# Kernel optimization log

Hardware: AMD Instinct MI355X
Metric: run time of the kernel (lower is better)

Reference implementation:

```python
import jax, jax.numpy as jnp
import numpy as np

N_NODES = 100000
N_EDGES = 1600000
N_GRAPHS = 256
F_NODE, F_EDGE, HID, OUT = 64, 16, 128, 128
BN_SCALE = 1.0 / np.sqrt(1.0 + 1e-5)  # BatchNorm eval with running mean 0, var 1


def setup_inputs() -> dict:
    key = jax.random.key(0)
    ks = iter(jax.random.split(key, 64))
    inp = {}
    inp["x"] = jax.random.normal(next(ks), (N_NODES, F_NODE), dtype=jnp.float32)
    inp["edge_attr"] = jax.random.normal(next(ks), (N_EDGES, F_EDGE), dtype=jnp.float32)
    inp["edge_index"] = jax.random.randint(next(ks), (2, N_EDGES), 0, N_NODES)
    inp["batch"] = jnp.sort(jax.random.randint(next(ks), (N_NODES,), 0, N_GRAPHS))

    def p(shape, scale):
        return (jax.random.normal(next(ks), shape, dtype=jnp.float32) * scale)

    in_dims = [F_NODE, HID, HID]
    for i, d in enumerate(in_dims):
        inp[f"el_w{i}"] = p((F_EDGE, d), F_EDGE ** -0.5)
        inp[f"el_b{i}"] = jnp.zeros((d,), jnp.float32)
        inp[f"c{i}_w1"] = p((d, HID), d ** -0.5)
        inp[f"c{i}_b1"] = jnp.zeros((HID,), jnp.float32)
        inp[f"c{i}_g"] = jnp.ones((HID,), jnp.float32)
        inp[f"c{i}_bt"] = jnp.zeros((HID,), jnp.float32)
        inp[f"c{i}_w2"] = p((HID, HID), HID ** -0.5)
        inp[f"c{i}_b2"] = jnp.zeros((HID,), jnp.float32)
    inp["o_w1"] = p((HID, OUT), HID ** -0.5)
    inp["o_b1"] = jnp.zeros((OUT,), jnp.float32)
    inp["o_w2"] = p((OUT, OUT), OUT ** -0.5)
    inp["o_b2"] = jnp.zeros((OUT,), jnp.float32)
    return inp


def reference(x, edge_attr,
              el_w0, el_b0, c0_w1, c0_b1, c0_g, c0_bt, c0_w2, c0_b2,
              el_w1, el_b1, c1_w1, c1_b1, c1_g, c1_bt, c1_w2, c1_b2,
              el_w2, el_b2, c2_w1, c2_b1, c2_g, c2_bt, c2_w2, c2_b2,
              o_w1, o_b1, o_w2, o_b2,
              edge_index, batch):
    src, dst = edge_index[0], edge_index[1]
    n = x.shape[0]
    layers = [
        (el_w0, el_b0, c0_w1, c0_b1, c0_g, c0_bt, c0_w2, c0_b2),
        (el_w1, el_b1, c1_w1, c1_b1, c1_g, c1_bt, c1_w2, c1_b2),
        (el_w2, el_b2, c2_w1, c2_b1, c2_g, c2_bt, c2_w2, c2_b2),
    ]
    h = x
    for (ew, eb, w1, b1, g, bt, w2, b2) in layers:
        ea = edge_attr @ ew + eb                              # [E, d]
        msg = jax.nn.relu(h[src] + ea)                        # GINEConv message
        agg = jax.ops.segment_sum(msg, dst, num_segments=n)   # scatter-sum to targets
        hh = h + agg                                          # (1+eps)*x + aggr, eps=0
        hh = hh @ w1 + b1                                     # MLP: Linear
        hh = g * (hh * BN_SCALE) + bt                         # BatchNorm1d (eval)
        hh = jax.nn.relu(hh)
        hh = hh @ w2 + b2                                     # MLP: Linear
        h = jax.nn.relu(hh)                                   # dropout(p=0, eval) + act
    s = jax.ops.segment_sum(h, batch, num_segments=N_GRAPHS)
    cnt = jax.ops.segment_sum(jnp.ones((n,), h.dtype), batch, num_segments=N_GRAPHS)
    pooled = s / jnp.maximum(cnt, 1.0)[:, None]               # scatter-mean pooling
    out = jax.nn.relu(pooled @ o_w1 + o_b1) @ o_w2 + o_b2     # out_lin
    return out
```

## Files before the change

### kernel.cpp

```cpp
#include <hip/hip_runtime.h>
#include <hip/hip_fp16.h>
#include <cstdint>
#include <cstddef>

#define N_NODES_C  100000
#define N_EDGES_C  1600000
#define N_GRAPHS_C 256
#define HID_C      128
#define BN_SCALE_C 0.9999950000374997f

#define SCAN_B 1024
#define SCAN_NB ((N_NODES_C + SCAN_B - 1) / SCAN_B)

typedef _Float16 h2 __attribute__((ext_vector_type(2)));
typedef _Float16 h4 __attribute__((ext_vector_type(4)));
typedef _Float16 h8 __attribute__((ext_vector_type(8)));
typedef float    f4 __attribute__((ext_vector_type(4)));

struct __align__(16) EA8 { h2 p[4]; };
struct __align__(8)  HQ  { h2 a, b; };
struct __align__(16) H8  { __half2 v[4]; };

#if defined(__has_builtin)
#  if __has_builtin(__builtin_amdgcn_fdot2)
#    define HAVE_FDOT2 1
#  endif
#endif
#ifndef HAVE_FDOT2
#  define HAVE_FDOT2 0
#endif

__device__ __forceinline__ float fdot2_(h2 a, h2 b, float c)
{
#if HAVE_FDOT2
    return __builtin_amdgcn_fdot2(a, b, c, false);
#else
    return c + (float)a[0] * (float)b[0] + (float)a[1] * (float)b[1];
#endif
}

__global__ __launch_bounds__(256) void hist_kernel(
    const int* __restrict__ dst, int* __restrict__ counts, int n_edges)
{
    int e = blockIdx.x * 256 + threadIdx.x;
    if (e < n_edges) atomicAdd(&counts[dst[e]], 1);
}

__global__ __launch_bounds__(SCAN_B) void scan1_kernel(
    const int* __restrict__ counts, int* __restrict__ incl,
    int* __restrict__ blocksums, int n)
{
    __shared__ int sdata[SCAN_B];
    const int lid = threadIdx.x;
    const int i = blockIdx.x * SCAN_B + lid;
    sdata[lid] = (i < n) ? counts[i] : 0;
    __syncthreads();
#pragma unroll
    for (int off = 1; off < SCAN_B; off <<= 1) {
        int t = (lid >= off) ? sdata[lid - off] : 0;
        __syncthreads();
        sdata[lid] += t;
        __syncthreads();
    }
    if (i < n) incl[i] = sdata[lid];
    if (lid == SCAN_B - 1) blocksums[blockIdx.x] = sdata[lid];
}

__global__ void scan2_kernel(const int* __restrict__ blocksums,
                             int* __restrict__ blockoffs, int nb)
{
    if (threadIdx.x == 0 && blockIdx.x == 0) {
        int off = 0;
        for (int b = 0; b < nb; ++b) { blockoffs[b] = off; off += blocksums[b]; }
    }
}

__global__ __launch_bounds__(SCAN_B) void scan3_kernel(
    int* __restrict__ incl, const int* __restrict__ blockoffs, int n)
{
    const int i = blockIdx.x * SCAN_B + threadIdx.x;
    if (i < n) incl[i] += blockoffs[blockIdx.x];
}

__global__ __launch_bounds__(256) void initrows_kernel(
    const int* __restrict__ incl, const int* __restrict__ counts,
    int* __restrict__ rowstart, int* __restrict__ cursor, int n)
{
    const int i = blockIdx.x * 256 + threadIdx.x;
    if (i < n) {
        const int rs = incl[i] - counts[i];
        rowstart[i] = rs;
        cursor[i]   = rs;
    }
}

__global__ __launch_bounds__(256) void scatter_kernel(
    const int* __restrict__ src, const int* __restrict__ dst,
    int* __restrict__ cursor, int* __restrict__ perm_src,
    int* __restrict__ perm_eid, int n_edges)
{
    const int e = blockIdx.x * 256 + threadIdx.x;
    if (e < n_edges) {
        const int pos = atomicAdd(&cursor[dst[e]], 1);
        perm_src[pos] = src[e];
        perm_eid[pos] = e;
    }
}

__global__ __launch_bounds__(256) void permute_ea_f16_kernel(
    const float* __restrict__ edge_attr, const int* __restrict__ perm_eid,
    __half* __restrict__ ea_f16, int n_edges)
{
    const int j = blockIdx.x * 256 + threadIdx.x;
    if (j >= n_edges) return;
    const int eid = perm_eid[j];
    const float4* p = (const float4*)(edge_attr + (size_t)eid * 16);
    const float4 q0 = p[0], q1 = p[1], q2 = p[2], q3 = p[3];
    H8 a, b;
    a.v[0] = __floats2half2_rn(q0.x, q0.y);
    a.v[1] = __floats2half2_rn(q0.z, q0.w);
    a.v[2] = __floats2half2_rn(q1.x, q1.y);
    a.v[3] = __floats2half2_rn(q1.z, q1.w);
    b.v[0] = __floats2half2_rn(q2.x, q2.y);
    b.v[1] = __floats2half2_rn(q2.z, q2.w);
    b.v[2] = __floats2half2_rn(q3.x, q3.y);
    b.v[3] = __floats2half2_rn(q3.z, q3.w);
    H8* o = (H8*)(ea_f16 + (size_t)j * 16);
    o[0] = a;
    o[1] = b;
}

__global__ __launch_bounds__(256) void cast_f16_kernel(
    const float* __restrict__ in, _Float16* __restrict__ out, int n4)
{
    const int i = blockIdx.x * 256 + threadIdx.x;
    if (i >= n4) return;
    const float4 v = ((const float4*)in)[i];
    h4 o; o[0] = (_Float16)v.x; o[1] = (_Float16)v.y;
    o[2] = (_Float16)v.z; o[3] = (_Float16)v.w;
    *(h4*)(out + (size_t)i * 4) = o;
}

__global__ __launch_bounds__(256) void transpose_w_kernel(
    const float* __restrict__ w, _Float16* __restrict__ wt, int K, int N)
{
    const int i = blockIdx.x * 256 + threadIdx.x;
    if (i >= K * N) return;
    const int n = i / K;
    const int k = i - n * K;
    wt[(size_t)n * K + k] = (_Float16)w[(size_t)k * N + n];
}

__device__ __forceinline__ float4 eamlp2(const EA8 a0, const EA8 c0,
                                         const h2 (*ew2h)[4], const float4 ebv)
{
    float4 m = {ebv.x, ebv.y, ebv.z, ebv.w};
#pragma unroll
    for (int k = 0; k < 4; ++k) {
        m.x = fdot2_(a0.p[k], ew2h[k][0], m.x);
        m.y = fdot2_(a0.p[k], ew2h[k][1], m.y);
        m.z = fdot2_(a0.p[k], ew2h[k][2], m.z);
        m.w = fdot2_(a0.p[k], ew2h[k][3], m.w);
    }
#pragma unroll
    for (int k = 0; k < 4; ++k) {
        m.x = fdot2_(c0.p[k], ew2h[4 + k][0], m.x);
        m.y = fdot2_(c0.p[k], ew2h[4 + k][1], m.y);
        m.z = fdot2_(c0.p[k], ew2h[4 + k][2], m.z);
        m.w = fdot2_(c0.p[k], ew2h[4 + k][3], m.w);
    }
    return m;
}

template<int DIN>
__global__ __launch_bounds__(256) void gine_agg_kernel(
    const _Float16* __restrict__ hin, const _Float16* __restrict__ ea16,
    const int* __restrict__ perm_src,
    const int* __restrict__ rowstart, const int* __restrict__ rowend,
    const float* __restrict__ ew, const float* __restrict__ eb,
    _Float16* __restrict__ x16, int n_nodes)
{
    constexpr int NQ    = DIN / 4;
    constexpr int SLOTS = 256 / NQ;
    const int fq   = threadIdx.x & (NQ - 1);
    const int slot = threadIdx.x / NQ;
    const int v = blockIdx.x * SLOTS + slot;
    if (v >= n_nodes) return;

    h2 ew2h[8][4];
#pragma unroll
    for (int k2 = 0; k2 < 8; ++k2)
#pragma unroll
        for (int fi = 0; fi < 4; ++fi) {
            h2 t;
            t[0] = (_Float16)ew[(size_t)(2 * k2)     * DIN + fq * 4 + fi];
            t[1] = (_Float16)ew[(size_t)(2 * k2 + 1) * DIN + fq * 4 + fi];
            ew2h[k2][fi] = t;
        }
    const float4 ebv = *(const float4*)(eb + fq * 4);

    const int s0 = rowstart[v];
    const int s1 = rowend[v];

    float4 acc = {0.f, 0.f, 0.f, 0.f};
    int j = s0;

    for (; j + 4 <= s1; j += 4) {
        const int sn0 = perm_src[j + 0];
        const int sn1 = perm_src[j + 1];
        const int sn2 = perm_src[j + 2];
        const int sn3 = perm_src[j + 3];
        const EA8* pe = (const EA8*)(ea16 + (size_t)j * 16);
        const EA8 a0 = pe[0], c0 = pe[1], a1 = pe[2], c1 = pe[3];
        const EA8 a2 = pe[4], c2 = pe[5], a3 = pe[6], c3 = pe[7];
        const HQ hq0 = *(const HQ*)(hin + (size_t)sn0 * DIN + fq * 4);
        const HQ hq1 = *(const HQ*)(hin + (size_t)sn1 * DIN + fq * 4);
        const HQ hq2 = *(const HQ*)(hin + (size_t)sn2 * DIN + fq * 4);
        const HQ hq3 = *(const HQ*)(hin + (size_t)sn3 * DIN + fq * 4);

        const float4 m0 = eamlp2(a0, c0, ew2h, ebv);
        const float4 m1 = eamlp2(a1, c1, ew2h, ebv);
        const float4 m2 = eamlp2(a2, c2, ew2h, ebv);
        const float4 m3 = eamlp2(a3, c3, ew2h, ebv);

        acc.x += fmaxf(m0.x + (float)hq0.a[0], 0.f) + fmaxf(m1.x + (float)hq1.a[0], 0.f)
               + fmaxf(m2.x + (float)hq2.a[0], 0.f) + fmaxf(m3.x + (float)hq3.a[0], 0.f);
        acc.y += fmaxf(m0.y + (float)hq0.a[1], 0.f) + fmaxf(m1.y + (float)hq1.a[1], 0.f)
               + fmaxf(m2.y + (float)hq2.a[1], 0.f) + fmaxf(m3.y + (float)hq3.a[1], 0.f);
        acc.z += fmaxf(m0.z + (float)hq0.b[0], 0.f) + fmaxf(m1.z + (float)hq1.b[0], 0.f)
               + fmaxf(m2.z + (float)hq2.b[0], 0.f) + fmaxf(m3.z + (float)hq3.b[0], 0.f);
        acc.w += fmaxf(m0.w + (float)hq0.b[1], 0.f) + fmaxf(m1.w + (float)hq1.b[1], 0.f)
               + fmaxf(m2.w + (float)hq2.b[1], 0.f) + fmaxf(m3.w + (float)hq3.b[1], 0.f);
    }
    if (j + 2 <= s1) {
        const int sn0 = perm_src[j + 0];
        const int sn1 = perm_src[j + 1];
        const EA8* pe = (const EA8*)(ea16 + (size_t)j * 16);
        const EA8 a0 = pe[0], c0 = pe[1], a1 = pe[2], c1 = pe[3];
        const HQ hq0 = *(const HQ*)(hin + (size_t)sn0 * DIN + fq * 4);
        const HQ hq1 = *(const HQ*)(hin + (size_t)sn1 * DIN + fq * 4);
        const float4 m0 = eamlp2(a0, c0, ew2h, ebv);
        const float4 m1 = eamlp2(a1, c1, ew2h, ebv);
        acc.x += fmaxf(m0.x + (float)hq0.a[0], 0.f) + fmaxf(m1.x + (float)hq1.a[0], 0.f);
        acc.y += fmaxf(m0.y + (float)hq0.a[1], 0.f) + fmaxf(m1.y + (float)hq1.a[1], 0.f);
        acc.z += fmaxf(m0.z + (float)hq0.b[0], 0.f) + fmaxf(m1.z + (float)hq1.b[0], 0.f);
        acc.w += fmaxf(m0.w + (float)hq0.b[1], 0.f) + fmaxf(m1.w + (float)hq1.b[1], 0.f);
        j += 2;
    }
    if (j < s1) {
        const int sn = perm_src[j];
        const EA8* pe = (const EA8*)(ea16 + (size_t)j * 16);
        const EA8 a0 = pe[0], c0 = pe[1];
        const HQ hq = *(const HQ*)(hin + (size_t)sn * DIN + fq * 4);
        const float4 m0 = eamlp2(a0, c0, ew2h, ebv);
        acc.x += fmaxf(m0.x + (float)hq.a[0], 0.f);
        acc.y += fmaxf(m0.y + (float)hq.a[1], 0.f);
        acc.z += fmaxf(m0.z + (float)hq.b[0], 0.f);
        acc.w += fmaxf(m0.w + (float)hq.b[1], 0.f);
    }

    const HQ hv = *(const HQ*)(hin + (size_t)v * DIN + fq * 4);
    h4 o;
    o[0] = (_Float16)(acc.x + (float)hv.a[0]);
    o[1] = (_Float16)(acc.y + (float)hv.a[1]);
    o[2] = (_Float16)(acc.z + (float)hv.b[0]);
    o[3] = (_Float16)(acc.w + (float)hv.b[1]);
    *(h4*)(x16 + (size_t)v * DIN + fq * 4) = o;
}

template<int DIN, bool LASTL>
__global__ __launch_bounds__(64) void node_mfma_kernel(
    const _Float16* __restrict__ x16,
    const _Float16* __restrict__ w1t, const float* __restrict__ b1,
    const float* __restrict__ gm, const float* __restrict__ bt,
    const _Float16* __restrict__ w2t, const float* __restrict__ b2,
    float* __restrict__ hout, _Float16* __restrict__ h16out, int n_tiles)
{
    constexpr int STP = HID_C + 8;
    __shared__ _Float16 s_t[16][STP];

    const int lane = threadIdx.x;
    const int tile = blockIdx.x;
    const int node0 = tile * 16;
    const int ln   = lane & 15;
    const int quad = lane >> 4;

    constexpr int NKS = DIN / 32;
    h8 af[NKS];
#pragma unroll
    for (int ks = 0; ks < NKS; ++ks)
        af[ks] = *(const h8*)(x16 + (size_t)(node0 + ln) * DIN + ks * 32 + quad * 8);

#pragma unroll
    for (int nt = 0; nt < 8; ++nt) {
        const int col = nt * 16 + ln;
        const float bv = b1[col];
        f4 acc = {bv, bv, bv, bv};
#pragma unroll
        for (int ks = 0; ks < NKS; ++ks) {
            const h8 bf = *(const h8*)(w1t + (size_t)col * DIN + ks * 32 + quad * 8);
            acc = __builtin_amdgcn_mfma_f32_16x16x32_f16(af[ks], bf, acc, 0, 0, 0);
        }
        const float gv = gm[col], btv = bt[col];
#pragma unroll
        for (int r = 0; r < 4; ++r) {
            const float t = fmaxf(fmaf(acc[r] * BN_SCALE_C, gv, btv), 0.f);
            s_t[quad * 4 + r][col] = (_Float16)t;
        }
    }
    __syncthreads();

    h8 af2[4];
#pragma unroll
    for (int ks = 0; ks < 4; ++ks)
        af2[ks] = *(const h8*)&s_t[ln][ks * 32 + quad * 8];

#pragma unroll
    for (int nt = 0; nt < 8; ++nt) {
        const int col = nt * 16 + ln;
        const float bv = b2[col];
        f4 acc = {bv, bv, bv, bv};
#pragma unroll
        for (int ks = 0; ks < 4; ++ks) {
            const h8 bf = *(const h8*)(w2t + (size_t)col * HID_C + ks * 32 + quad * 8);
            acc = __builtin_amdgcn_mfma_f32_16x16x32_f16(af2[ks], bf, acc, 0, 0, 0);
        }
#pragma unroll
        for (int r = 0; r < 4; ++r) {
            const int node = node0 + quad * 4 + r;
            const float v = fmaxf(acc[r], 0.f);
            if (LASTL) {
                hout[(size_t)node * HID_C + col] = v;
            } else {
                h16out[(size_t)node * HID_C + col] = (_Float16)v;
            }
        }
    }
}

__global__ __launch_bounds__(256) void pool_kernel(
    const float* __restrict__ hfin, const int* __restrict__ batch,
    const float* __restrict__ w1, const float* __restrict__ b1,
    const float* __restrict__ w2, const float* __restrict__ b2,
    float* __restrict__ out, int n_nodes)
{
    const int gid = blockIdx.x;

    int lo = 0, hi = n_nodes;
    while (lo < hi) { int mid = (lo + hi) >> 1; if (batch[mid] < gid) lo = mid + 1; else hi = mid; }
    const int start = lo;
    hi = n_nodes;
    while (lo < hi) { int mid = (lo + hi) >> 1; if (batch[mid] < gid + 1) lo = mid + 1; else hi = mid; }
    const int end = lo;

    const int f = threadIdx.x & (HID_C - 1);
    const int half = threadIdx.x >> 7;

    float sum = 0.f;
    for (int n = start + half; n < end; n += 2)
        sum += hfin[(size_t)n * HID_C + f];

    __shared__ float s_sum[2][HID_C];
    __shared__ float s_p[HID_C];
    __shared__ float s_t[HID_C];
    s_sum[half][f] = sum;
    __syncthreads();

    if (threadIdx.x < HID_C) {
        const float cnt = (float)(end - start);
        s_p[f] = (s_sum[0][f] + s_sum[1][f]) / fmaxf(cnt, 1.f);
    }
    __syncthreads();

    if (threadIdx.x < HID_C) {
        float acc = b1[f];
        for (int k = 0; k < HID_C; ++k) acc = fmaf(s_p[k], w1[k * HID_C + f], acc);
        s_t[f] = fmaxf(acc, 0.f);
    }
    __syncthreads();

    if (threadIdx.x < HID_C) {
        float acc = b2[f];
        for (int k = 0; k < HID_C; ++k) acc = fmaf(s_t[k], w2[k * HID_C + f], acc);
        out[(size_t)gid * HID_C + f] = acc;
    }
}

extern "C" void kernel_launch(void* const* d_in, const int* in_sizes, int n_in,
                              void* d_out, int out_size, void* d_ws, size_t ws_size,
                              hipStream_t stream)
{
    const float* x         = (const float*)d_in[0];
    const float* edge_attr = (const float*)d_in[1];
    const int*   edge_index= (const int*)  d_in[2];
    const int*   batch     = (const int*)  d_in[3];
    const int*   src = edge_index;
    const int*   dst = edge_index + N_EDGES_C;

    const float* el_w[3] = {(const float*)d_in[4],  (const float*)d_in[12], (const float*)d_in[20]};
    const float* el_b[3] = {(const float*)d_in[5],  (const float*)d_in[13], (const float*)d_in[21]};
    const float* c_w1[3] = {(const float*)d_in[6],  (const float*)d_in[14], (const float*)d_in[22]};
    const float* c_b1[3] = {(const float*)d_in[7],  (const float*)d_in[15], (const float*)d_in[23]};
    const float* c_g [3] = {(const float*)d_in[8],  (const float*)d_in[16], (const float*)d_in[24]};
    const float* c_bt[3] = {(const float*)d_in[9],  (const float*)d_in[17], (const float*)d_in[25]};
    const float* c_w2[3] = {(const float*)d_in[10], (const float*)d_in[18], (const float*)d_in[26]};
    const float* c_b2[3] = {(const float*)d_in[11], (const float*)d_in[19], (const float*)d_in[27]};
    const float* o_w1 = (const float*)d_in[28];
    const float* o_b1 = (const float*)d_in[29];
    const float* o_w2 = (const float*)d_in[30];
    const float* o_b2 = (const float*)d_in[31];

    char* wsp = (char*)d_ws;
    size_t used = 0;
    auto alloc = [&](size_t bytes) { char* p = wsp + used; used += (bytes + 255) & ~(size_t)255; return p; };
    float* h        = (float*)alloc((size_t)N_NODES_C * HID_C * 4);
    int*   counts   = (int*)alloc((size_t)N_NODES_C * 4);
    int*   incl     = (int*)alloc((size_t)N_NODES_C * 4);
    int*   rowstart = (int*)alloc((size_t)N_NODES_C * 4);
    int*   cursor   = (int*)alloc((size_t)N_NODES_C * 4);
    int*   blocksums= (int*)alloc(128 * 4);
    int*   blockoffs= (int*)alloc(128 * 4);
    int*   perm_src = (int*)alloc((size_t)N_EDGES_C * 4);
    int*   perm_eid = (int*)alloc((size_t)N_EDGES_C * 4);
    _Float16* ea_f16 = (_Float16*)alloc((size_t)N_EDGES_C * 16 * 2);
    _Float16* x16    = (_Float16*)alloc((size_t)N_NODES_C * HID_C * 2);
    _Float16* h16_a  = (_Float16*)alloc((size_t)N_NODES_C * HID_C * 2);
    _Float16* h16_b  = (_Float16*)alloc((size_t)N_NODES_C * HID_C * 2);
    _Float16* x_f16  = (_Float16*)alloc((size_t)N_NODES_C * 64 * 2);
    _Float16* w1t[3], *w2t[3];
    for (int l = 0; l < 3; ++l) {
        w1t[l] = (_Float16*)alloc((size_t)HID_C * HID_C * 2);
        w2t[l] = (_Float16*)alloc((size_t)HID_C * HID_C * 2);
    }
    (void)ws_size;

    hipMemsetAsync(counts, 0, (size_t)N_NODES_C * 4, stream);
    hist_kernel<<<(N_EDGES_C + 255) / 256, 256, 0, stream>>>(dst, counts, N_EDGES_C);
    scan1_kernel<<<SCAN_NB, SCAN_B, 0, stream>>>(counts, incl, blocksums, N_NODES_C);
    scan2_kernel<<<1, 64, 0, stream>>>(blocksums, blockoffs, SCAN_NB);
    scan3_kernel<<<SCAN_NB, SCAN_B, 0, stream>>>(incl, blockoffs, N_NODES_C);
    initrows_kernel<<<(N_NODES_C + 255) / 256, 256, 0, stream>>>(incl, counts, rowstart,
                                                                 cursor, N_NODES_C);
    scatter_kernel<<<(N_EDGES_C + 255) / 256, 256, 0, stream>>>(src, dst, cursor,
                                                                perm_src, perm_eid, N_EDGES_C);
    permute_ea_f16_kernel<<<(N_EDGES_C + 255) / 256, 256, 0, stream>>>(
        edge_attr, perm_eid, (__half*)ea_f16, N_EDGES_C);
    cast_f16_kernel<<<(N_NODES_C * 64 / 4 + 255) / 256, 256, 0, stream>>>(
        x, x_f16, N_NODES_C * 64 / 4);
    for (int l = 0; l < 3; ++l) {
        const int K1 = (l == 0) ? 64 : HID_C;
        transpose_w_kernel<<<(K1 * HID_C + 255) / 256, 256, 0, stream>>>(
            c_w1[l], w1t[l], K1, HID_C);
        transpose_w_kernel<<<(HID_C * HID_C + 255) / 256, 256, 0, stream>>>(
            c_w2[l], w2t[l], HID_C, HID_C);
    }

    const int n_tiles = N_NODES_C / 16;

    gine_agg_kernel<64><<<(N_NODES_C + 15) / 16, 256, 0, stream>>>(
        x_f16, ea_f16, perm_src, rowstart, incl, el_w[0], el_b[0],
        x16, N_NODES_C);
    node_mfma_kernel<64, false><<<n_tiles, 64, 0, stream>>>(
        x16, w1t[0], c_b1[0], c_g[0], c_bt[0], w2t[0], c_b2[0],
        h, h16_a, n_tiles);
    gine_agg_kernel<128><<<(N_NODES_C + 7) / 8, 256, 0, stream>>>(
        h16_a, ea_f16, perm_src, rowstart, incl, el_w[1], el_b[1],
        x16, N_NODES_C);
    node_mfma_kernel<128, false><<<n_tiles, 64, 0, stream>>>(
        x16, w1t[1], c_b1[1], c_g[1], c_bt[1], w2t[1], c_b2[1],
        h, h16_b, n_tiles);
    gine_agg_kernel<128><<<(N_NODES_C + 7) / 8, 256, 0, stream>>>(
        h16_b, ea_f16, perm_src, rowstart, incl, el_w[2], el_b[2],
        x16, N_NODES_C);
    node_mfma_kernel<128, true><<<n_tiles, 64, 0, stream>>>(
        x16, w1t[2], c_b1[2], c_g[2], c_bt[2], w2t[2], c_b2[2],
        h, h16_a, n_tiles);

    pool_kernel<<<N_GRAPHS_C, 256, 0, stream>>>(h, batch, o_w1, o_b1, o_w2, o_b2,
                                                (float*)d_out, N_NODES_C);
}
```

Measured before the change: 0.9998 ms.

## Prepack edge weights, unroll gather by eight, batch four MFMA tiles per block

Edge-MLP weights are converted to fp16 and packed per feature quad once in a new pack kernel, so each agg thread loads them with vector reads instead of 32 strided scalar fp32 loads and conversions. The edge loop is unrolled to 8 edges with all neighbour gathers issued first and edge attributes read through nontemporal loads, and the self-feature load is moved ahead of the loop. The node MFMA kernel now runs four wavefronts (four tiles) per 256-thread block with per-wave shared tiles, reducing block count. The new weight setup contains a leftover first unpack loop that is immediately overwritten, and the larger unroll raises register pressure.

After: 1.273 ms. 27.4% more time.

```diff
diff --git a/kernel.cpp b/kernel.cpp
--- a/kernel.cpp
+++ b/kernel.cpp
@@ -151,25 +151,71 @@
     wt[(size_t)n * K + k] = (_Float16)w[(size_t)k * N + n];
 }
 
-__device__ __forceinline__ float4 eamlp2(const EA8 a0, const EA8 c0,
-                                         const h2 (*ew2h)[4], const float4 ebv)
-{
+__global__ __launch_bounds__(256) void pack_ew_kernel(
+    const float* __restrict__ ew, h2* __restrict__ out, int din)
+{
+    const int i = blockIdx.x * 256 + threadIdx.x;
+    const int total = din * 8;
+    if (i >= total) return;
+    const int fq = i >> 5, r = i & 31, k2 = r >> 2, fi = r & 3;
+    const int f = fq * 4 + fi;
+    h2 t;
+    t[0] = (_Float16)ew[(size_t)(2 * k2)     * din + f];
+    t[1] = (_Float16)ew[(size_t)(2 * k2 + 1) * din + f];
+    out[i] = t;
+}
+
+__device__ __forceinline__ float4 eamlp2(const h8 a8, const h8 c8,
+                                         const h2 (&ew2h)[8][4], const float4 ebv)
+{
+    h2 ap[4], cp[4];
+#pragma unroll
+    for (int k = 0; k < 4; ++k) {
+        ap[k][0] = a8[2 * k]; ap[k][1] = a8[2 * k + 1];
+        cp[k][0] = c8[2 * k]; cp[k][1] = c8[2 * k + 1];
+    }
     float4 m = {ebv.x, ebv.y, ebv.z, ebv.w};
 #pragma unroll
     for (int k = 0; k < 4; ++k) {
-        m.x = fdot2_(a0.p[k], ew2h[k][0], m.x);
-        m.y = fdot2_(a0.p[k], ew2h[k][1], m.y);
-        m.z = fdot2_(a0.p[k], ew2h[k][2], m.z);
-        m.w = fdot2_(a0.p[k], ew2h[k][3], m.w);
+        m.x = fdot2_(ap[k], ew2h[k][0], m.x);
+        m.y = fdot2_(ap[k], ew2h[k][1], m.y);
+        m.z = fdot2_(ap[k], ew2h[k][2], m.z);
+        m.w = fdot2_(ap[k], ew2h[k][3], m.w);
     }
 #pragma unroll
     for (int k = 0; k < 4; ++k) {
-        m.x = fdot2_(c0.p[k], ew2h[4 + k][0], m.x);
-        m.y = fdot2_(c0.p[k], ew2h[4 + k][1], m.y);
-        m.z = fdot2_(c0.p[k], ew2h[4 + k][2], m.z);
-        m.w = fdot2_(c0.p[k], ew2h[4 + k][3], m.w);
+        m.x = fdot2_(cp[k], ew2h[4 + k][0], m.x);
+        m.y = fdot2_(cp[k], ew2h[4 + k][1], m.y);
+        m.z = fdot2_(cp[k], ew2h[4 + k][2], m.z);
+        m.w = fdot2_(cp[k], ew2h[4 + k][3], m.w);
     }
     return m;
+}
+
+template<int DIN, int U>
+__device__ __forceinline__ void agg_edges(
+    const _Float16* __restrict__ hin, const _Float16* __restrict__ ea16,
+    const int* __restrict__ perm_src, int j, int fq,
+    const h2 (&ew2h)[8][4], const float4 ebv, float4& acc)
+{
+    int sn[U];
+#pragma unroll
+    for (int u = 0; u < U; ++u) sn[u] = perm_src[j + u];
+    HQ hq[U];
+#pragma unroll
+    for (int u = 0; u < U; ++u)
+        hq[u] = *(const HQ*)(hin + (size_t)sn[u] * DIN + fq * 4);
+#pragma unroll
+    for (int u = 0; u < U; ++u) {
+        const h8* pe = (const h8*)(ea16 + (size_t)(j + u) * 16);
+        const h8 a = __builtin_nontemporal_load(pe);
+        const h8 c = __builtin_nontemporal_load(pe + 1);
+        const float4 m = eamlp2(a, c, ew2h, ebv);
+        acc.x += fmaxf(m.x + (float)hq[u].a[0], 0.f);
+        acc.y += fmaxf(m.y + (float)hq[u].a[1], 0.f);
+        acc.z += fmaxf(m.z + (float)hq[u].b[0], 0.f);
+        acc.w += fmaxf(m.w + (float)hq[u].b[1], 0.f);
+    }
 }
 
 template<int DIN>
@@ -177,7 +223,7 @@
     const _Float16* __restrict__ hin, const _Float16* __restrict__ ea16,
     const int* __restrict__ perm_src,
     const int* __restrict__ rowstart, const int* __restrict__ rowend,
-    const float* __restrict__ ew, const float* __restrict__ eb,
+    const h2* __restrict__ ew16, const float* __restrict__ eb,
     _Float16* __restrict__ x16, int n_nodes)
 {
     constexpr int NQ    = DIN / 4;
@@ -187,79 +233,50 @@
     const int v = blockIdx.x * SLOTS + slot;
     if (v >= n_nodes) return;
 
+    h8 w0 = *(const h8*)(ew16 + (size_t)fq * 32);
+    h8 w1 = *(const h8*)(ew16 + (size_t)fq * 32 + 4);
+    h8 w2 = *(const h8*)(ew16 + (size_t)fq * 32 + 8);
+    h8 w3 = *(const h8*)(ew16 + (size_t)fq * 32 + 12);
     h2 ew2h[8][4];
 #pragma unroll
-    for (int k2 = 0; k2 < 8; ++k2)
-#pragma unroll
-        for (int fi = 0; fi < 4; ++fi) {
-            h2 t;
-            t[0] = (_Float16)ew[(size_t)(2 * k2)     * DIN + fq * 4 + fi];
-            t[1] = (_Float16)ew[(size_t)(2 * k2 + 1) * DIN + fq * 4 + fi];
-            ew2h[k2][fi] = t;
+    for (int r = 0; r < 4; ++r) {
+        const h8 wv = (r == 0) ? w0 : (r == 1) ? w1 : (r == 2) ? w2 : w3;
+#pragma unroll
+        for (int c = 0; c < 4; ++c) {
+            h2 t; t[0] = wv[2 * c]; t[1] = wv[2 * c + 1];
+            ew2h[r * 2 + (c >> 1)][(c & 1) * 2 + 0] = t;
         }
+    }
+    {
+        const h2* wl = (const h2*)(ew16 + (size_t)fq * 32);
+#pragma unroll
+        for (int k2 = 0; k2 < 8; ++k2)
+#pragma unroll
+            for (int fi = 0; fi < 4; ++fi)
+                ew2h[k2][fi] = wl[k2 * 4 + fi];
+    }
     const float4 ebv = *(const float4*)(eb + fq * 4);
 
     const int s0 = rowstart[v];
     const int s1 = rowend[v];
 
+    const HQ hv = *(const HQ*)(hin + (size_t)v * DIN + fq * 4);
+
     float4 acc = {0.f, 0.f, 0.f, 0.f};
     int j = s0;
-
-    for (; j + 4 <= s1; j += 4) {
-        const int sn0 = perm_src[j + 0];
-        const int sn1 = perm_src[j + 1];
-        const int sn2 = perm_src[j + 2];
-        const int sn3 = perm_src[j + 3];
-        const EA8* pe = (const EA8*)(ea16 + (size_t)j * 16);
-        const EA8 a0 = pe[0], c0 = pe[1], a1 = pe[2], c1 = pe[3];
-        const EA8 a2 = pe[4], c2 = pe[5], a3 = pe[6], c3 = pe[7];
-        const HQ hq0 = *(const HQ*)(hin + (size_t)sn0 * DIN + fq * 4);
-        const HQ hq1 = *(const HQ*)(hin + (size_t)sn1 * DIN + fq * 4);
-        const HQ hq2 = *(const HQ*)(hin + (size_t)sn2 * DIN + fq * 4);
-        const HQ hq3 = *(const HQ*)(hin + (size_t)sn3 * DIN + fq * 4);
-
-        const float4 m0 = eamlp2(a0, c0, ew2h, ebv);
-        const float4 m1 = eamlp2(a1, c1, ew2h, ebv);
-        const float4 m2 = eamlp2(a2, c2, ew2h, ebv);
-        const float4 m3 = eamlp2(a3, c3, ew2h, ebv);
-
-        acc.x += fmaxf(m0.x + (float)hq0.a[0], 0.f) + fmaxf(m1.x + (float)hq1.a[0], 0.f)
-               + fmaxf(m2.x + (float)hq2.a[0], 0.f) + fmaxf(m3.x + (float)hq3.a[0], 0.f);
-        acc.y += fmaxf(m0.y + (float)hq0.a[1], 0.f) + fmaxf(m1.y + (float)hq1.a[1], 0.f)
-               + fmaxf(m2.y + (float)hq2.a[1], 0.f) + fmaxf(m3.y + (float)hq3.a[1], 0.f);
-        acc.z += fmaxf(m0.z + (float)hq0.b[0], 0.f) + fmaxf(m1.z + (float)hq1.b[0], 0.f)
-               + fmaxf(m2.z + (float)hq2.b[0], 0.f) + fmaxf(m3.z + (float)hq3.b[0], 0.f);
-        acc.w += fmaxf(m0.w + (float)hq0.b[1], 0.f) + fmaxf(m1.w + (float)hq1.b[1], 0.f)
-               + fmaxf(m2.w + (float)hq2.b[1], 0.f) + fmaxf(m3.w + (float)hq3.b[1], 0.f);
+    for (; j + 8 <= s1; j += 8)
+        agg_edges<DIN, 8>(hin, ea16, perm_src, j, fq, ew2h, ebv, acc);
+    if (j + 4 <= s1) {
+        agg_edges<DIN, 4>(hin, ea16, perm_src, j, fq, ew2h, ebv, acc);
+        j += 4;
     }
     if (j + 2 <= s1) {
-        const int sn0 = perm_src[j + 0];
-        const int sn1 = perm_src[j + 1];
-        const EA8* pe = (const EA8*)(ea16 + (size_t)j * 16);
-        const EA8 a0 = pe[0], c0 = pe[1], a1 = pe[2], c1 = pe[3];
-        const HQ hq0 = *(const HQ*)(hin + (size_t)sn0 * DIN + fq * 4);
-        const HQ hq1 = *(const HQ*)(hin + (size_t)sn1 * DIN + fq * 4);
-        const float4 m0 = eamlp2(a0, c0, ew2h, ebv);
-        const float4 m1 = eamlp2(a1, c1, ew2h, ebv);
-        acc.x += fmaxf(m0.x + (float)hq0.a[0], 0.f) + fmaxf(m1.x + (float)hq1.a[0], 0.f);
-        acc.y += fmaxf(m0.y + (float)hq0.a[1], 0.f) + fmaxf(m1.y + (float)hq1.a[1], 0.f);
-        acc.z += fmaxf(m0.z + (float)hq0.b[0], 0.f) + fmaxf(m1.z + (float)hq1.b[0], 0.f);
-        acc.w += fmaxf(m0.w + (float)hq0.b[1], 0.f) + fmaxf(m1.w + (float)hq1.b[1], 0.f);
+        agg_edges<DIN, 2>(hin, ea16, perm_src, j, fq, ew2h, ebv, acc);
         j += 2;
     }
-    if (j < s1) {
-        const int sn = perm_src[j];
-        const EA8* pe = (const EA8*)(ea16 + (size_t)j * 16);
-        const EA8 a0 = pe[0], c0 = pe[1];
-        const HQ hq = *(const HQ*)(hin + (size_t)sn * DIN + fq * 4);
-        const float4 m0 = eamlp2(a0, c0, ew2h, ebv);
-        acc.x += fmaxf(m0.x + (float)hq.a[0], 0.f);
-        acc.y += fmaxf(m0.y + (float)hq.a[1], 0.f);
-        acc.z += fmaxf(m0.z + (float)hq.b[0], 0.f);
-        acc.w += fmaxf(m0.w + (float)hq.b[1], 0.f);
-    }
-
-    const HQ hv = *(const HQ*)(hin + (size_t)v * DIN + fq * 4);
+    if (j < s1)
+        agg_edges<DIN, 1>(hin, ea16, perm_src, j, fq, ew2h, ebv, acc);
+
     h4 o;
     o[0] = (_Float16)(acc.x + (float)hv.a[0]);
     o[1] = (_Float16)(acc.y + (float)hv.a[1]);
@@ -269,7 +286,7 @@
 }
 
 template<int DIN, bool LASTL>
-__global__ __launch_bounds__(64) void node_mfma_kernel(
+__global__ __launch_bounds__(256) void node_mfma_kernel(
     const _Float16* __restrict__ x16,
     const _Float16* __restrict__ w1t, const float* __restrict__ b1,
     const float* __restrict__ gm, const float* __restrict__ bt,
@@ -277,10 +294,12 @@
     float* __restrict__ hout, _Float16* __restrict__ h16out, int n_tiles)
 {
     constexpr int STP = HID_C + 8;
-    __shared__ _Float16 s_t[16][STP];
-
-    const int lane = threadIdx.x;
-    const int tile = blockIdx.x;
+    __shared__ _Float16 s_t[4][16][STP];
+
+    const int w    = threadIdx.x >> 6;
+    const int lane = threadIdx.x & 63;
+    int tile = blockIdx.x * 4 + w;
+    if (tile >= n_tiles) tile = n_tiles - 1;
     const int node0 = tile * 16;
     const int ln   = lane & 15;
     const int quad = lane >> 4;
@@ -305,7 +324,7 @@
 #pragma unroll
         for (int r = 0; r < 4; ++r) {
             const float t = fmaxf(fmaf(acc[r] * BN_SCALE_C, gv, btv), 0.f);
-            s_t[quad * 4 + r][col] = (_Float16)t;
+            s_t[w][quad * 4 + r][col] = (_Float16)t;
         }
     }
     __syncthreads();
@@ -313,7 +332,7 @@
     h8 af2[4];
 #pragma unroll
     for (int ks = 0; ks < 4; ++ks)
-        af2[ks] = *(const h8*)&s_t[ln][ks * 32 + quad * 8];
+        af2[ks] = *(const h8*)&s_t[w][ln][ks * 32 + quad * 8];
 
 #pragma unroll
     for (int nt = 0; nt < 8; ++nt) {
@@ -428,9 +447,11 @@
     _Float16* h16_b  = (_Float16*)alloc((size_t)N_NODES_C * HID_C * 2);
     _Float16* x_f16  = (_Float16*)alloc((size_t)N_NODES_C * 64 * 2);
     _Float16* w1t[3], *w2t[3];
+    h2* ew16p[3];
     for (int l = 0; l < 3; ++l) {
         w1t[l] = (_Float16*)alloc((size_t)HID_C * HID_C * 2);
         w2t[l] = (_Float16*)alloc((size_t)HID_C * HID_C * 2);
+        ew16p[l] = (h2*)alloc((size_t)HID_C * 8 * 4);
     }
     (void)ws_size;
 
@@ -453,26 +474,30 @@
             c_w1[l], w1t[l], K1, HID_C);
         transpose_w_kernel<<<(HID_C * HID_C + 255) / 256, 256, 0, stream>>>(
             c_w2[l], w2t[l], HID_C, HID_C);
+        const int din = (l == 0) ? 64 : HID_C;
+        pack_ew_kernel<<<(din * 8 + 255) / 256, 256, 0, stream>>>(
+            el_w[l], ew16p[l], din);
     }
 
     const int n_tiles = N_NODES_C / 16;
+    const int nb_node = (n_tiles + 3) / 4;
 
     gine_agg_kernel<64><<<(N_NODES_C + 15) / 16, 256, 0, stream>>>(
-        x_f16, ea_f16, perm_src, rowstart, incl, el_w[0], el_b[0],
+        x_f16, ea_f16, perm_src, rowstart, incl, ew16p[0], el_b[0],
         x16, N_NODES_C);
-    node_mfma_kernel<64, false><<<n_tiles, 64, 0, stream>>>(
+    node_mfma_kernel<64, false><<<nb_node, 256, 0, stream>>>(
         x16, w1t[0], c_b1[0], c_g[0], c_bt[0], w2t[0], c_b2[0],
         h, h16_a, n_tiles);
     gine_agg_kernel<128><<<(N_NODES_C + 7) / 8, 256, 0, stream>>>(
-        h16_a, ea_f16, perm_src, rowstart, incl, el_w[1], el_b[1],
+        h16_a, ea_f16, perm_src, rowstart, incl, ew16p[1], el_b[1],
         x16, N_NODES_C);
-    node_mfma_kernel<128, false><<<n_tiles, 64, 0, stream>>>(
+    node_mfma_kernel<128, false><<<nb_node, 256, 0, stream>>>(
         x16, w1t[1], c_b1[1], c_g[1], c_bt[1], w2t[1], c_b2[1],
         h, h16_b, n_tiles);
     gine_agg_kernel<128><<<(N_NODES_C + 7) / 8, 256, 0, stream>>>(
-        h16_b, ea_f16, perm_src, rowstart, incl, el_w[2], el_b[2],
+        h16_b, ea_f16, perm_src, rowstart, incl, ew16p[2], el_b[2],
         x16, N_NODES_C);
-    node_mfma_kernel<128, true><<<n_tiles, 64, 0, stream>>>(
+    node_mfma_kernel<128, true><<<nb_node, 256, 0, stream>>>(
         x16, w1t[2], c_b1[2], c_g[2], c_bt[2], w2t[2], c_b2[2],
         h, h16_a, n_tiles);
 
```
